# Optimization experiments

Hardware: AMD Instinct MI355X
Metric: run time of the kernel (lower is better)

Reference implementation:

```python
import jax, jax.numpy as jnp
import numpy as np

SCENE_BOUND = 1.5
INV_SCALE = 1.0 / (2.0 * np.sqrt(2.0))  # (1/sqrt(2))^3 per 3D haar synthesis step


def idwt3_haar(approx, details):
    """One level of 3D inverse Haar DWT.

    approx:  (C, D, D, D)   'aaa' subband
    details: (7, C, D, D, D) subbands in ptwt key order
             ('aad','ada','add','daa','dad','dda','ddd')
    returns: (C, 2D, 2D, 2D)
    """
    C, D = approx.shape[0], approx.shape[1]
    # Stack 8 subbands; key order is lexicographic in (a=0, d=1) per axis,
    # so reshape to a (2,2,2) subband grid indexed (b_depth, b_height, b_width).
    coeffs = jnp.concatenate([approx[None], details], axis=0).reshape(2, 2, 2, C, D, D, D)
    # Haar synthesis signs: approx contributes +1 to both output phases,
    # detail contributes +1 to even phase, -1 to odd phase.
    S = jnp.array([[1.0, 1.0], [1.0, -1.0]], dtype=approx.dtype)
    out = jnp.einsum('uvwcijk,up,vq,wr->cipjqkr', coeffs, S, S, S) * jnp.asarray(INV_SCALE, approx.dtype)
    return out.reshape(C, 2 * D, 2 * D, 2 * D)


def trilinear_query(vol, xyz, bound):
    """torch grid_sample(mode='bilinear', padding='zeros', align_corners=True).

    vol: (C, R, R, R) with dims (D, H, W); xyz: (N, 3) world coords,
    columns (x, y, z) index (W, H, D) respectively.
    returns: (N, C)
    """
    C, R = vol.shape[0], vol.shape[1]
    g = xyz / bound                                # normalized to [-1, 1]
    pix = (g + 1.0) * 0.5 * (R - 1)                # align_corners=True mapping
    i0 = jnp.floor(pix).astype(jnp.int32)
    frac = pix - i0.astype(vol.dtype)
    x0, y0, z0 = i0[:, 0], i0[:, 1], i0[:, 2]
    fx, fy, fz = frac[:, 0], frac[:, 1], frac[:, 2]

    def gather(ix, iy, iz):
        valid = ((ix >= 0) & (ix < R) & (iy >= 0) & (iy < R) & (iz >= 0) & (iz < R))
        v = vol[:, jnp.clip(iz, 0, R - 1), jnp.clip(iy, 0, R - 1), jnp.clip(ix, 0, R - 1)]  # (C, N)
        return v * valid.astype(vol.dtype)

    out = jnp.zeros((C, xyz.shape[0]), dtype=vol.dtype)
    for dz in (0, 1):
        wz = fz if dz else 1.0 - fz
        for dy in (0, 1):
            wy = fy if dy else 1.0 - fy
            for dx in (0, 1):
                wx = fx if dx else 1.0 - fx
                out = out + gather(x0 + dx, y0 + dy, z0 + dz) * (wx * wy * wz)
    return out.T  # (N, C)


def setup_inputs() -> dict:
    key = jax.random.key(0)
    k0, k1, k2, k3, k4 = jax.random.split(key, 5)
    C = 28
    approx = jax.random.normal(k0, (C, 16, 16, 16), dtype=jnp.float32) * 0.01
    details_0 = jax.random.normal(k1, (7, C, 16, 16, 16), dtype=jnp.float32) * 0.001
    details_1 = jax.random.normal(k2, (7, C, 32, 32, 32), dtype=jnp.float32) * 0.001
    details_2 = jax.random.normal(k3, (7, C, 64, 64, 64), dtype=jnp.float32) * 0.001
    xyz = (jax.random.uniform(k4, (1_000_000, 3), dtype=jnp.float32) * 2.0 - 1.0) * SCENE_BOUND
    return {"approx": approx, "details_0": details_0, "details_1": details_1,
            "details_2": details_2, "xyz": xyz}


def reference(approx, details_0, details_1, details_2, xyz):
    # reconstruct(max_level=None): incremental multi-level IDWT synthesis
    vol = approx
    for d in (details_0, details_1, details_2):
        vol = idwt3_haar(vol, d)          # (C, 32^3) -> (C, 64^3) -> (C, 128^3)
    # query(): trilinear interpolation at world-space points
    return trilinear_query(vol, xyz, SCENE_BOUND)  # (N, C)
```

## Files before the change

### kernel.cpp

```cpp
#include <hip/hip_runtime.h>
#include <hip/hip_fp16.h>

#define INVS 0.35355339059327373f
#define CCH 28
#define QRS 127
#define CAP 256

typedef float f32x4 __attribute__((ext_vector_type(4)));

__device__ __forceinline__ void haar8(const float c[8], float o[8]) {
    float t00p = c[0] + c[1], t00m = c[0] - c[1];
    float t01p = c[2] + c[3], t01m = c[2] - c[3];
    float t10p = c[4] + c[5], t10m = c[4] - c[5];
    float t11p = c[6] + c[7], t11m = c[6] - c[7];
    float u00p = t00p + t01p, u00m = t00m + t01m;
    float u01p = t00p - t01p, u01m = t00m - t01m;
    float u10p = t10p + t11p, u10m = t10m + t11m;
    float u11p = t10p - t11p, u11m = t10m - t11m;
    o[0] = (u00p + u10p) * INVS;  o[1] = (u00m + u10m) * INVS;
    o[2] = (u01p + u11p) * INVS;  o[3] = (u01m + u11m) * INVS;
    o[4] = (u00p - u10p) * INVS;  o[5] = (u00m - u10m) * INVS;
    o[6] = (u01p - u11p) * INVS;  o[7] = (u01m - u11m) * INVS;
}

__device__ __forceinline__ float3 pixcoord(float x, float y, float z) {
    const float R1 = 63.5f, IB = 1.0f / 1.5f;
    float3 p;
    p.x = __fmul_rn(__fadd_rn(__fmul_rn(x, IB), 1.0f), R1);
    p.y = __fmul_rn(__fadd_rn(__fmul_rn(y, IB), 1.0f), R1);
    p.z = __fmul_rn(__fadd_rn(__fmul_rn(z, IB), 1.0f), R1);
    return p;
}
__device__ __forceinline__ int cell_of(float3 p) {
    int cx = min(max((int)floorf(p.x), 0), 127) >> 3;
    int cy = min(max((int)floorf(p.y), 0), 127) >> 3;
    int cz = min(max((int)floorf(p.z), 0), 127) >> 2;
    return (cz * 16 + cy) * 16 + cx;
}

__global__ void __launch_bounds__(64) idwt01(const float* __restrict__ approx,
                                             const float* __restrict__ det0,
                                             const float* __restrict__ det1,
                                             __half* __restrict__ vol1) {
    constexpr int D03 = 16 * 16 * 16, D13 = 32 * 32 * 32;
    int t = blockIdx.x * 64 + threadIdx.x;
    int x0 = t & 15, y0 = (t >> 4) & 15, z0 = (t >> 8) & 15, c = t >> 12;
    int base0 = c * D03 + ((z0 * 16 + y0) * 16 + x0);
    float cf[8];
    cf[0] = approx[base0];
#pragma unroll
    for (int j = 0; j < 7; ++j) cf[j + 1] = det0[j * (CCH * D03) + base0];
    float v0[8];
    haar8(cf, v0);
    unsigned int hbuf[4][4][2];
#pragma unroll
    for (int p = 0; p < 2; ++p)
#pragma unroll
        for (int q = 0; q < 2; ++q)
#pragma unroll
            for (int r = 0; r < 2; ++r) {
                int z1 = 2 * z0 + p, y1 = 2 * y0 + q, x1 = 2 * x0 + r;
                int base1 = c * D13 + ((z1 * 32 + y1) * 32 + x1);
                float cg[8];
                cg[0] = v0[p * 4 + q * 2 + r];
#pragma unroll
                for (int j = 0; j < 7; ++j) cg[j + 1] = det1[j * (CCH * D13) + base1];
                float o[8];
                haar8(cg, o);
#pragma unroll
                for (int sz = 0; sz < 2; ++sz)
#pragma unroll
                    for (int sy = 0; sy < 2; ++sy) {
                        __half2 h;
                        h.x = __float2half(o[sz * 4 + sy * 2 + 0]);
                        h.y = __float2half(o[sz * 4 + sy * 2 + 1]);
                        hbuf[2 * p + sz][2 * q + sy][r] = *(unsigned int*)&h;
                    }
            }
#pragma unroll
    for (int pz = 0; pz < 4; ++pz)
#pragma unroll
        for (int py = 0; py < 4; ++py) {
            uint2 v;
            v.x = hbuf[pz][py][0];
            v.y = hbuf[pz][py][1];
            long oi = (((long)(c * 64 + 4 * z0 + pz) * 64 + (4 * y0 + py)) * 64 + 4 * x0) >> 2;
            ((uint2*)vol1)[oi] = v;
        }
}

__global__ void __launch_bounds__(256) idwt_last(const __half* __restrict__ vol1,
                                                 const float* __restrict__ details,
                                                 __half* __restrict__ out) {
    constexpr int D3 = 64 * 64 * 64;
    __shared__ unsigned int lds4[4 * CCH * 65];
    unsigned short* lds = (unsigned short*)lds4;
    int zc = blockIdx.x >> 6, yc = blockIdx.x & 63;
    int rowc = (zc * 64 + yc) * 64;
    int xc = threadIdx.x & 63, cg = threadIdx.x >> 6;
#pragma unroll
    for (int k = 0; k < 7; ++k) {
        int c = cg + 4 * k;
        int base = c * D3 + rowc + xc;
        float cf[8];
        cf[0] = (float)vol1[base];
#pragma unroll
        for (int j = 0; j < 7; ++j) cf[j + 1] = details[j * (CCH * D3) + base];
        float o[8];
        haar8(cf, o);
#pragma unroll
        for (int m = 0; m < 4; ++m) {
            __half2 h;
            h.x = __float2half(o[2 * m]);
            h.y = __float2half(o[2 * m + 1]);
            lds4[(m * CCH + c) * 65 + xc] = *(unsigned int*)&h;
        }
    }
    __syncthreads();
#pragma unroll
    for (int it = 0; it < 7; ++it) {
        int t2 = it * 256 + threadIdx.x;
        int plane = t2 / 448;
        int rem = t2 - plane * 448;
        int p = plane >> 1, q = plane & 1;
        unsigned int h[8];
#pragma unroll
        for (int j = 0; j < 8; ++j) {
            int f = rem * 8 + j;
            int vox = f / 28;
            int ch = f - 28 * vox;
            h[j] = lds[(plane * CCH + ch) * 130 + vox];
        }
        uint4 r4;
        r4.x = h[0] | (h[1] << 16);
        r4.y = h[2] | (h[3] << 16);
        r4.z = h[4] | (h[5] << 16);
        r4.w = h[6] | (h[7] << 16);
        long orow = ((long)(2 * zc + p) * 128 + (2 * yc + q)) * (128 * CCH);
        ((uint4*)(out + orow))[rem] = r4;
    }
}

__global__ void scatter_k(const float* __restrict__ xyz, int* __restrict__ cursor,
                          unsigned int* __restrict__ recs, const __half* __restrict__ vol,
                          float* __restrict__ out, int N) {
    int i = blockIdx.x * 256 + threadIdx.x;
    if (i >= N) return;
    float3 p = pixcoord(xyz[3 * i], xyz[3 * i + 1], xyz[3 * i + 2]);
    int cell = cell_of(p);
    int pos = atomicAdd(&cursor[cell], 1);
    if (pos < CAP) {
        recs[cell * CAP + pos] = (unsigned int)i;
        return;
    }
    float flx = floorf(p.x), fly = floorf(p.y), flz = floorf(p.z);
    int ix0 = (int)flx, iy0 = (int)fly, iz0 = (int)flz;
    float fx = p.x - flx, fy = p.y - fly, fz = p.z - flz;
    float acc[CCH];
#pragma unroll
    for (int k = 0; k < CCH; ++k) acc[k] = 0.0f;
    for (int dz = 0; dz < 2; ++dz) {
        int iz = iz0 + dz;
        bool vz = (iz >= 0) & (iz < 128);
        float wz = dz ? fz : 1.0f - fz;
        int gz = min(max(iz, 0), 127);
        for (int dy = 0; dy < 2; ++dy) {
            int iy = iy0 + dy;
            bool vy = (iy >= 0) & (iy < 128);
            float wy = dy ? fy : 1.0f - fy;
            int gy = min(max(iy, 0), 127);
            for (int dx = 0; dx < 2; ++dx) {
                int ix = ix0 + dx;
                bool vx = (ix >= 0) & (ix < 128);
                float wx = dx ? fx : 1.0f - fx;
                int gx = min(max(ix, 0), 127);
                float w = (vx & vy & vz) ? (wx * wy * wz) : 0.0f;
                const uint2* pv = (const uint2*)(vol + ((long)(gz * 128 + gy) * 128 + gx) * CCH);
#pragma unroll
                for (int j = 0; j < 7; ++j) {
                    uint2 u = pv[j];
                    float2 f0 = __half22float2(*(__half2*)&u.x);
                    float2 f1 = __half22float2(*(__half2*)&u.y);
                    acc[4 * j + 0] += w * f0.x;
                    acc[4 * j + 1] += w * f0.y;
                    acc[4 * j + 2] += w * f1.x;
                    acc[4 * j + 3] += w * f1.y;
                }
            }
        }
    }
#pragma unroll
    for (int k = 0; k < CCH; ++k) out[(long)i * CCH + k] = acc[k];
}

__global__ void __launch_bounds__(256, 7) query_cell(const unsigned int* __restrict__ recs,
                                                     const int* __restrict__ cursor,
                                                     const float* __restrict__ xyz,
                                                     const __half* __restrict__ vol,
                                                     float* __restrict__ out) {
    __shared__ unsigned int lds[45 * QRS];
    int cell = blockIdx.x;
    int cx = cell & 15, cy = (cell >> 4) & 15, cz = cell >> 8;
    const unsigned int* vd = (const unsigned int*)vol;
    const long VOLDW = 128L * 128 * 128 * 14;
    for (int e = threadIdx.x; e < 45 * 63; e += 256) {
        int row = e / 63;
        int k2  = e - row * 63;
        int lz = row / 9, ly = row - 9 * lz;
        int gz = min(4 * cz + lz, 127), gy = min(8 * cy + ly, 127);
        long g = ((long)(gz * 128 + gy) * 128 + 8 * cx) * 14 + 2 * k2;
        g = min(g, VOLDW - 2);
        uint2 v = *(const uint2*)(vd + g);
        lds[row * QRS + 2 * k2]     = v.x;
        lds[row * QRS + 2 * k2 + 1] = v.y;
    }
    __syncthreads();
    int cnt = min(cursor[cell], CAP);
    for (int k = threadIdx.x; k < cnt; k += 256) {
        int q = (int)recs[cell * CAP + k];
        float xq = xyz[3 * q], yq = xyz[3 * q + 1], zq = xyz[3 * q + 2];
        float3 p = pixcoord(xq, yq, zq);
        float px = p.x, py = p.y, pz = p.z;
        float flx = floorf(px), fly = floorf(py), flz = floorf(pz);
        int ix0 = (int)flx, iy0 = (int)fly, iz0 = (int)flz;
        float fx = px - flx, fy = py - fly, fz = pz - flz;
        float acc[CCH];
#pragma unroll
        for (int k2 = 0; k2 < CCH; ++k2) acc[k2] = 0.0f;
#pragma unroll
        for (int dz = 0; dz < 2; ++dz) {
            int iz = iz0 + dz;
            bool vz = (iz >= 0) & (iz < 128);
            float wz = dz ? fz : 1.0f - fz;
            int lzc = min(max(iz, 0), 127) - 4 * cz;
#pragma unroll
            for (int dy = 0; dy < 2; ++dy) {
                int iy = iy0 + dy;
                bool vy = (iy >= 0) & (iy < 128);
                float wy = dy ? fy : 1.0f - fy;
                int lyc = min(max(iy, 0), 127) - 8 * cy;
#pragma unroll
                for (int dx = 0; dx < 2; ++dx) {
                    int ix = ix0 + dx;
                    bool vx = (ix >= 0) & (ix < 128);
                    float wx = dx ? fx : 1.0f - fx;
                    int lxc = min(max(ix, 0), 127) - 8 * cx;
                    float w = (vx & vy & vz) ? (wx * wy * wz) : 0.0f;
                    const unsigned int* pr = &lds[(lzc * 9 + lyc) * QRS + 14 * lxc];
#pragma unroll
                    for (int j = 0; j < 7; ++j) {
                        unsigned int u0 = pr[2 * j], u1 = pr[2 * j + 1];
                        float2 f0 = __half22float2(*(__half2*)&u0);
                        float2 f1 = __half22float2(*(__half2*)&u1);
                        acc[4 * j + 0] += w * f0.x;
                        acc[4 * j + 1] += w * f0.y;
                        acc[4 * j + 2] += w * f1.x;
                        acc[4 * j + 3] += w * f1.y;
                    }
                }
            }
        }
        f32x4* o4 = (f32x4*)(out + (long)q * CCH);
#pragma unroll
        for (int j = 0; j < 7; ++j) {
            f32x4 v = {acc[4 * j], acc[4 * j + 1], acc[4 * j + 2], acc[4 * j + 3]};
            o4[j] = v;
        }
    }
}

extern "C" void kernel_launch(void* const* d_in, const int* in_sizes, int n_in,
                              void* d_out, int out_size, void* d_ws, size_t ws_size,
                              hipStream_t stream) {
    const float* approx = (const float*)d_in[0];
    const float* det0   = (const float*)d_in[1];
    const float* det1   = (const float*)d_in[2];
    const float* det2   = (const float*)d_in[3];
    const float* xyz    = (const float*)d_in[4];
    int N = in_sizes[4] / 3;

    char* ws = (char*)d_ws;
    __half*       vol1 = (__half*)ws;
    __half*       vol2 = (__half*)(ws + 14680064);
    int*          curs = (int*)(ws + 132120576);
    unsigned int* recs = (unsigned int*)(ws + 132153344);

    hipMemsetAsync(curs, 0, 8192 * sizeof(int), stream);
    idwt01<<<1792, 64, 0, stream>>>(approx, det0, det1, vol1);
    idwt_last<<<4096, 256, 0, stream>>>(vol1, det2, vol2);
    int nb = (N + 255) / 256;
    scatter_k<<<nb, 256, 0, stream>>>(xyz, curs, recs, vol2, (float*)d_out, N);
    query_cell<<<8192, 256, 0, stream>>>(recs, curs, xyz, vol2, (float*)d_out);
}
```

Measured before the change: 517.4 us.

## Pad volume channels to 32, drop LDS tiling in query, fold cursor memset

```diff
diff --git a/kernel.cpp b/kernel.cpp
--- a/kernel.cpp
+++ b/kernel.cpp
@@ -3,7 +3,7 @@
 
 #define INVS 0.35355339059327373f
 #define CCH 28
-#define QRS 127
+#define VSTR 32
 #define CAP 256
 
 typedef float f32x4 __attribute__((ext_vector_type(4)));
@@ -38,54 +38,53 @@
     return (cz * 16 + cy) * 16 + cx;
 }
 
-__global__ void __launch_bounds__(64) idwt01(const float* __restrict__ approx,
-                                             const float* __restrict__ det0,
-                                             const float* __restrict__ det1,
-                                             __half* __restrict__ vol1) {
+__global__ void __launch_bounds__(256) idwt01(const float* __restrict__ approx,
+                                              const float* __restrict__ det0,
+                                              const float* __restrict__ det1,
+                                              __half* __restrict__ vol1,
+                                              int* __restrict__ curs) {
     constexpr int D03 = 16 * 16 * 16, D13 = 32 * 32 * 32;
-    int t = blockIdx.x * 64 + threadIdx.x;
-    int x0 = t & 15, y0 = (t >> 4) & 15, z0 = (t >> 8) & 15, c = t >> 12;
-    int base0 = c * D03 + ((z0 * 16 + y0) * 16 + x0);
+    int t = blockIdx.x * 256 + threadIdx.x;
+    if (t < 8192) curs[t] = 0;
+    int xp = t & 15;
+    int y1 = (t >> 4) & 31;
+    int z1 = (t >> 9) & 31;
+    int c  = t >> 14;
+    int base0 = c * D03 + (((z1 >> 1) * 16 + (y1 >> 1)) * 16 + xp);
     float cf[8];
     cf[0] = approx[base0];
 #pragma unroll
     for (int j = 0; j < 7; ++j) cf[j + 1] = det0[j * (CCH * D03) + base0];
     float v0[8];
     haar8(cf, v0);
-    unsigned int hbuf[4][4][2];
+    int sub = (z1 & 1) * 4 + (y1 & 1) * 2;
+    int base1 = c * D13 + ((z1 * 32 + y1) * 32 + 2 * xp);
+    float cfA[8], cfB[8];
+    cfA[0] = v0[sub];
+    cfB[0] = v0[sub + 1];
+#pragma unroll
+    for (int j = 0; j < 7; ++j) {
+        float2 d2 = *(const float2*)(det1 + j * (CCH * D13) + base1);
+        cfA[j + 1] = d2.x;
+        cfB[j + 1] = d2.y;
+    }
+    float oA[8], oB[8];
+    haar8(cfA, oA);
+    haar8(cfB, oB);
+    uint2* outv = (uint2*)vol1;
 #pragma unroll
     for (int p = 0; p < 2; ++p)
 #pragma unroll
-        for (int q = 0; q < 2; ++q)
-#pragma unroll
-            for (int r = 0; r < 2; ++r) {
-                int z1 = 2 * z0 + p, y1 = 2 * y0 + q, x1 = 2 * x0 + r;
-                int base1 = c * D13 + ((z1 * 32 + y1) * 32 + x1);
-                float cg[8];
-                cg[0] = v0[p * 4 + q * 2 + r];
-#pragma unroll
-                for (int j = 0; j < 7; ++j) cg[j + 1] = det1[j * (CCH * D13) + base1];
-                float o[8];
-                haar8(cg, o);
-#pragma unroll
-                for (int sz = 0; sz < 2; ++sz)
-#pragma unroll
-                    for (int sy = 0; sy < 2; ++sy) {
-                        __half2 h;
-                        h.x = __float2half(o[sz * 4 + sy * 2 + 0]);
-                        h.y = __float2half(o[sz * 4 + sy * 2 + 1]);
-                        hbuf[2 * p + sz][2 * q + sy][r] = *(unsigned int*)&h;
-                    }
-            }
-#pragma unroll
-    for (int pz = 0; pz < 4; ++pz)
-#pragma unroll
-        for (int py = 0; py < 4; ++py) {
+        for (int q = 0; q < 2; ++q) {
+            int k0 = p * 4 + q * 2;
+            __half2 lo, hi;
+            lo.x = __float2half(oA[k0]);     lo.y = __float2half(oA[k0 + 1]);
+            hi.x = __float2half(oB[k0]);     hi.y = __float2half(oB[k0 + 1]);
             uint2 v;
-            v.x = hbuf[pz][py][0];
-            v.y = hbuf[pz][py][1];
-            long oi = (((long)(c * 64 + 4 * z0 + pz) * 64 + (4 * y0 + py)) * 64 + 4 * x0) >> 2;
-            ((uint2*)vol1)[oi] = v;
+            v.x = *(unsigned int*)&lo;
+            v.y = *(unsigned int*)&hi;
+            long oi = (((long)(c * 64 + 2 * z1 + p) * 64 + 2 * y1 + q) * 64 + 4 * xp) >> 2;
+            outv[oi] = v;
         }
 }
 
@@ -118,25 +117,25 @@
     }
     __syncthreads();
 #pragma unroll
-    for (int it = 0; it < 7; ++it) {
+    for (int it = 0; it < 8; ++it) {
         int t2 = it * 256 + threadIdx.x;
-        int plane = t2 / 448;
-        int rem = t2 - plane * 448;
+        int plane = t2 >> 9;
+        int rem = t2 & 511;
         int p = plane >> 1, q = plane & 1;
+        int vox = rem >> 2;
+        int bc = (rem & 3) * 8;
         unsigned int h[8];
 #pragma unroll
         for (int j = 0; j < 8; ++j) {
-            int f = rem * 8 + j;
-            int vox = f / 28;
-            int ch = f - 28 * vox;
-            h[j] = lds[(plane * CCH + ch) * 130 + vox];
+            int ch = bc + j;
+            h[j] = (ch < CCH) ? (unsigned int)lds[(plane * CCH + ch) * 130 + vox] : 0u;
         }
         uint4 r4;
         r4.x = h[0] | (h[1] << 16);
         r4.y = h[2] | (h[3] << 16);
         r4.z = h[4] | (h[5] << 16);
         r4.w = h[6] | (h[7] << 16);
-        long orow = ((long)(2 * zc + p) * 128 + (2 * yc + q)) * (128 * CCH);
+        long orow = ((long)(2 * zc + p) * 128 + (2 * yc + q)) * (128L * VSTR);
         ((uint4*)(out + orow))[rem] = r4;
     }
 }
@@ -175,7 +174,7 @@
                 float wx = dx ? fx : 1.0f - fx;
                 int gx = min(max(ix, 0), 127);
                 float w = (vx & vy & vz) ? (wx * wy * wz) : 0.0f;
-                const uint2* pv = (const uint2*)(vol + ((long)(gz * 128 + gy) * 128 + gx) * CCH);
+                const uint2* pv = (const uint2*)(vol + (((long)(gz * 128 + gy) * 128 + gx) << 5));
 #pragma unroll
                 for (int j = 0; j < 7; ++j) {
                     uint2 u = pv[j];
@@ -193,79 +192,59 @@
     for (int k = 0; k < CCH; ++k) out[(long)i * CCH + k] = acc[k];
 }
 
-__global__ void __launch_bounds__(256, 7) query_cell(const unsigned int* __restrict__ recs,
-                                                     const int* __restrict__ cursor,
-                                                     const float* __restrict__ xyz,
-                                                     const __half* __restrict__ vol,
-                                                     float* __restrict__ out) {
-    __shared__ unsigned int lds[45 * QRS];
+__device__ __forceinline__ void fma14(float acc[CCH], uint4 a0, uint4 a1, uint4 a2, uint4 a3,
+                                      float w) {
+    unsigned int u[14] = {a0.x, a0.y, a0.z, a0.w, a1.x, a1.y, a1.z, a1.w,
+                          a2.x, a2.y, a2.z, a2.w, a3.x, a3.y};
+#pragma unroll
+    for (int d = 0; d < 14; ++d) {
+        float2 f = __half22float2(*(__half2*)&u[d]);
+        acc[2 * d]     += w * f.x;
+        acc[2 * d + 1] += w * f.y;
+    }
+}
+
+__global__ void __launch_bounds__(256) query_cell(const unsigned int* __restrict__ recs,
+                                                  const int* __restrict__ cursor,
+                                                  const float* __restrict__ xyz,
+                                                  const __half* __restrict__ vol,
+                                                  float* __restrict__ out) {
     int cell = blockIdx.x;
-    int cx = cell & 15, cy = (cell >> 4) & 15, cz = cell >> 8;
-    const unsigned int* vd = (const unsigned int*)vol;
-    const long VOLDW = 128L * 128 * 128 * 14;
-    for (int e = threadIdx.x; e < 45 * 63; e += 256) {
-        int row = e / 63;
-        int k2  = e - row * 63;
-        int lz = row / 9, ly = row - 9 * lz;
-        int gz = min(4 * cz + lz, 127), gy = min(8 * cy + ly, 127);
-        long g = ((long)(gz * 128 + gy) * 128 + 8 * cx) * 14 + 2 * k2;
-        g = min(g, VOLDW - 2);
-        uint2 v = *(const uint2*)(vd + g);
-        lds[row * QRS + 2 * k2]     = v.x;
-        lds[row * QRS + 2 * k2 + 1] = v.y;
-    }
-    __syncthreads();
+    int k = threadIdx.x;
     int cnt = min(cursor[cell], CAP);
-    for (int k = threadIdx.x; k < cnt; k += 256) {
-        int q = (int)recs[cell * CAP + k];
-        float xq = xyz[3 * q], yq = xyz[3 * q + 1], zq = xyz[3 * q + 2];
-        float3 p = pixcoord(xq, yq, zq);
-        float px = p.x, py = p.y, pz = p.z;
-        float flx = floorf(px), fly = floorf(py), flz = floorf(pz);
-        int ix0 = (int)flx, iy0 = (int)fly, iz0 = (int)flz;
-        float fx = px - flx, fy = py - fly, fz = pz - flz;
-        float acc[CCH];
-#pragma unroll
-        for (int k2 = 0; k2 < CCH; ++k2) acc[k2] = 0.0f;
-#pragma unroll
-        for (int dz = 0; dz < 2; ++dz) {
-            int iz = iz0 + dz;
-            bool vz = (iz >= 0) & (iz < 128);
-            float wz = dz ? fz : 1.0f - fz;
-            int lzc = min(max(iz, 0), 127) - 4 * cz;
-#pragma unroll
-            for (int dy = 0; dy < 2; ++dy) {
-                int iy = iy0 + dy;
-                bool vy = (iy >= 0) & (iy < 128);
-                float wy = dy ? fy : 1.0f - fy;
-                int lyc = min(max(iy, 0), 127) - 8 * cy;
-#pragma unroll
-                for (int dx = 0; dx < 2; ++dx) {
-                    int ix = ix0 + dx;
-                    bool vx = (ix >= 0) & (ix < 128);
-                    float wx = dx ? fx : 1.0f - fx;
-                    int lxc = min(max(ix, 0), 127) - 8 * cx;
-                    float w = (vx & vy & vz) ? (wx * wy * wz) : 0.0f;
-                    const unsigned int* pr = &lds[(lzc * 9 + lyc) * QRS + 14 * lxc];
-#pragma unroll
-                    for (int j = 0; j < 7; ++j) {
-                        unsigned int u0 = pr[2 * j], u1 = pr[2 * j + 1];
-                        float2 f0 = __half22float2(*(__half2*)&u0);
-                        float2 f1 = __half22float2(*(__half2*)&u1);
-                        acc[4 * j + 0] += w * f0.x;
-                        acc[4 * j + 1] += w * f0.y;
-                        acc[4 * j + 2] += w * f1.x;
-                        acc[4 * j + 3] += w * f1.y;
-                    }
-                }
-            }
-        }
-        f32x4* o4 = (f32x4*)(out + (long)q * CCH);
-#pragma unroll
-        for (int j = 0; j < 7; ++j) {
-            f32x4 v = {acc[4 * j], acc[4 * j + 1], acc[4 * j + 2], acc[4 * j + 3]};
-            o4[j] = v;
-        }
+    if (k >= cnt) return;
+    int q = (int)recs[cell * CAP + k];
+    float3 p = pixcoord(xyz[3 * q], xyz[3 * q + 1], xyz[3 * q + 2]);
+    float flx = floorf(p.x), fly = floorf(p.y), flz = floorf(p.z);
+    int ix0 = (int)flx, iy0 = (int)fly, iz0 = (int)flz;
+    float fx = p.x - flx, fy = p.y - fly, fz = p.z - flz;
+    int gx0 = min(max(ix0, 0), 127),     gy0 = min(max(iy0, 0), 127),     gz0 = min(max(iz0, 0), 127);
+    int gx1 = min(max(ix0 + 1, 0), 127), gy1 = min(max(iy0 + 1, 0), 127), gz1 = min(max(iz0 + 1, 0), 127);
+    float wx0 = (ix0 >= 0 && ix0 < 128) ? 1.0f - fx : 0.0f;
+    float wx1 = (ix0 + 1 >= 0 && ix0 + 1 < 128) ? fx : 0.0f;
+    float wy0 = (iy0 >= 0 && iy0 < 128) ? 1.0f - fy : 0.0f;
+    float wy1 = (iy0 + 1 >= 0 && iy0 + 1 < 128) ? fy : 0.0f;
+    float wz0 = (iz0 >= 0 && iz0 < 128) ? 1.0f - fz : 0.0f;
+    float wz1 = (iz0 + 1 >= 0 && iz0 + 1 < 128) ? fz : 0.0f;
+
+    float acc[CCH];
+#pragma unroll
+    for (int j = 0; j < CCH; ++j) acc[j] = 0.0f;
+#pragma unroll
+    for (int c8 = 0; c8 < 8; ++c8) {
+        int gx = (c8 & 1) ? gx1 : gx0;
+        int gy = (c8 & 2) ? gy1 : gy0;
+        int gz = (c8 & 4) ? gz1 : gz0;
+        float w = ((c8 & 1) ? wx1 : wx0) * ((c8 & 2) ? wy1 : wy0) * ((c8 & 4) ? wz1 : wz0);
+        const uint4* pv = (const uint4*)(vol + (((long)(gz * 128 + gy) * 128 + gx) << 5));
+        uint4 a0 = pv[0], a1 = pv[1], a2 = pv[2], a3 = pv[3];
+        fma14(acc, a0, a1, a2, a3, w);
+    }
+    f32x4* o4 = (f32x4*)(out + (long)q * CCH);
+#pragma unroll
+    for (int j = 0; j < 7; ++j) {
+        f32x4 v = {acc[4 * j], acc[4 * j + 1], acc[4 * j + 2], acc[4 * j + 3]};
+        o4[j] = v;
     }
 }
 
@@ -280,13 +259,12 @@
     int N = in_sizes[4] / 3;
 
     char* ws = (char*)d_ws;
-    __half*       vol1 = (__half*)ws;
-    __half*       vol2 = (__half*)(ws + 14680064);
-    int*          curs = (int*)(ws + 132120576);
-    unsigned int* recs = (unsigned int*)(ws + 132153344);
-
-    hipMemsetAsync(curs, 0, 8192 * sizeof(int), stream);
-    idwt01<<<1792, 64, 0, stream>>>(approx, det0, det1, vol1);
+    __half*       vol1  = (__half*)ws;
+    unsigned int* recs  = (unsigned int*)ws;
+    __half*       vol2  = (__half*)(ws + 14680064);
+    int*          curs  = (int*)(ws + 148897792);
+
+    idwt01<<<1792, 256, 0, stream>>>(approx, det0, det1, vol1, curs);
     idwt_last<<<4096, 256, 0, stream>>>(vol1, det2, vol2);
     int nb = (N + 255) / 256;
     scatter_k<<<nb, 256, 0, stream>>>(xyz, curs, recs, vol2, (float*)d_out, N);
```

After: 537.8 us. 3.9% more time.
